# Performance work log

Measured on AMD Instinct MI355X. Metric: run time of the kernel, lower is better.

## Reference

```python
import jax, jax.numpy as jnp
import numpy as np

B, T, C = 8, 2048, 512   # batch, seq_len, channels (= output_size for residual)
H, K, D = 4, 128, 128    # heads, key_size, per-head value size
KS, DIL = 4, 4           # conv kernel size, dilation = kernal_size**block_id
BAND = 3                 # matrix_band_part num_lower = num_upper = 3
NEG = -10000000.0


def setup_inputs() -> dict:
    key = jax.random.key(0)
    ks = jax.random.split(key, 12)
    s = 0.02
    f32 = jnp.float32
    x = jax.random.normal(ks[0], (B, T, C), f32)
    # per-head q/k/v dense params (stacked over head axis)
    Wq = jax.random.normal(ks[1], (H, C, K), f32) * s
    bq = jnp.zeros((H, K), f32)
    Wk = jax.random.normal(ks[2], (H, C, K), f32) * s
    bk = jnp.zeros((H, K), f32)
    Wv = jax.random.normal(ks[3], (H, C, D), f32) * s
    bv = jnp.zeros((H, D), f32)
    # output combiner Dense(output_size)
    Wo = jax.random.normal(ks[4], (H * D, C), f32) * s
    bo = jnp.zeros((C,), f32)
    # causal dilated Conv1D: kernel layout WIO = (kernel, in, out)
    Wc = jax.random.normal(ks[5], (KS, C, C), f32) * s
    bc = jnp.zeros((C,), f32)
    return {"x": x, "Wq": Wq, "bq": bq, "Wk": Wk, "bk": bk,
            "Wv": Wv, "bv": bv, "Wo": Wo, "bo": bo, "Wc": Wc, "bc": bc}


def reference(x, Wq, bq, Wk, bk, Wv, bv, Wo, bo, Wc, bc):
    # per-head projections: [B,H,T,K/D]
    q = jnp.einsum('btc,hck->bhtk', x, Wq) + bq[None, :, None, :]
    k = jnp.einsum('btc,hck->bhtk', x, Wk) + bk[None, :, None, :]
    v = jnp.einsum('btc,hcd->bhtd', x, Wv) + bv[None, :, None, :]
    # dense scores then band mask (faithful to matrix_band_part + abs>0 mask)
    sim = jnp.einsum('bhtk,bhsk->bhts', q, k) / jnp.sqrt(jnp.float32(K))
    idx = jnp.arange(T)
    band = (jnp.abs(idx[:, None] - idx[None, :]) <= BAND).astype(sim.dtype)
    simb = sim * band
    mask = jnp.where(jnp.abs(simb) > 0.0, 0.0, 1.0).astype(sim.dtype)
    att = jax.nn.softmax(simb + NEG * mask, axis=-1)
    heads = jnp.einsum('bhts,bhsd->bhtd', att, v)          # [B,H,T,D]
    cat = heads.transpose(0, 2, 1, 3).reshape(B, T, H * D)  # concat heads
    out = cat @ Wo + bo                                     # Dense(512)
    # causal dilated conv + relu
    pad = (KS - 1) * DIL
    conv = jax.lax.conv_general_dilated(
        out, Wc, window_strides=(1,), padding=[(pad, 0)],
        rhs_dilation=(DIL,), dimension_numbers=('NWC', 'WIO', 'NWC'))
    conv = jax.nn.relu(conv + bc)
    res = conv + x
    return jnp.where(res >= 0, res, 0.2 * res)  # leaky_relu(alpha=0.2)
```

## Files before the change

### kernel.cpp

```cpp
#include <hip/hip_runtime.h>
#include <math.h>

#define Bb    8
#define Tseq  2048
#define Cch   512
#define Mrows 16384
#define Nqkv  1536

typedef __bf16 bf16x8 __attribute__((ext_vector_type(8)));
typedef __bf16 bf16x4 __attribute__((ext_vector_type(4)));
typedef float  f32x4  __attribute__((ext_vector_type(4)));

__device__ __forceinline__ void gld_lds16(const void* g, void* l) {
  __builtin_amdgcn_global_load_lds(
      (const __attribute__((address_space(1))) unsigned int*)g,
      (__attribute__((address_space(3))) unsigned int*)l, 16, 0, 0);
}

#define SWZ(r, g) (((r) << 6) + ((((g) ^ ((r) & 7))) << 3))

__device__ __forceinline__ void swizzle_mn(int* m0, int* n0) {
  const int NX = gridDim.x;
  const int total = NX * gridDim.y;
  const int lid = blockIdx.y * NX + blockIdx.x;
  const int xcd = lid & 7;
  const int chunk = lid >> 3;
  const int idx = xcd * (total >> 3) + chunk;
  const int mt = idx / NX;
  const int nt = idx - mt * NX;
  *m0 = mt * 128;
  *n0 = nt * 128;
}

__global__ __launch_bounds__(256, 2) void gemm_qkv_wp_kernel(
    const __bf16* __restrict__ xb, const __bf16* __restrict__ Wqkv_t,
    const float* __restrict__ bq, const float* __restrict__ bk,
    const float* __restrict__ bv, __bf16* __restrict__ qkv,
    const __bf16* __restrict__ Wc_t, const __bf16* __restrict__ Wob,
    __bf16* __restrict__ Wp_bt) {
  __shared__ __align__(16) __bf16 As[2][128 * 64];
  __shared__ __align__(16) __bf16 Bs[2][128 * 64];
  const int tid = threadIdx.x;
  const int w = tid >> 6, lane = tid & 63;
  const int wm = w & 1, wn = w >> 1;
  const int lm = lane & 15, quad = lane >> 4;
  const int srow = lane >> 3;
  const int scol = (((lane & 7) ^ srow) << 3);
  const int lid = blockIdx.x;

  const __bf16 *Ap, *Bp;
  __bf16* op;
  int lda, ldo, m0, n0;
  bool dobias;
  if (lid < 1536) {
    const int xcd = lid & 7, chunk = lid >> 3;
    const int idx = xcd * 192 + chunk;
    const int mt = idx / 12, nt = idx - mt * 12;
    m0 = mt * 128; n0 = nt * 128;
    Ap = xb; lda = 512; Bp = Wqkv_t;
    op = qkv; ldo = 1536; dobias = true;
  } else {
    const int l2 = lid - 1536;
    const int z = l2 >> 4;
    m0 = ((l2 >> 2) & 3) * 128; n0 = (l2 & 3) * 128;
    Ap = Wc_t + z * 512; lda = 2048; Bp = Wob;
    op = Wp_bt + z * 512; ldo = 2048; dobias = false;
  }

  auto stage = [&](int buf, int k0) {
#pragma unroll
    for (int it = 0; it < 4; ++it) {
      const int c = w * 4 + it;
      const int row = c * 8 + srow;
      gld_lds16(Ap + (size_t)(m0 + row) * lda + k0 + scol, &As[buf][c * 512]);
      gld_lds16(Bp + (size_t)(n0 + row) * 512 + k0 + scol, &Bs[buf][c * 512]);
    }
  };

  f32x4 acc[4][4] = {};
  stage(0, 0);
  int cur = 0;
  for (int k0 = 0; k0 < 512; k0 += 64) {
    if (k0 + 64 < 512) {
      stage(cur ^ 1, k0 + 64);
      asm volatile("s_waitcnt vmcnt(8)" ::: "memory");
    } else {
      asm volatile("s_waitcnt vmcnt(0)" ::: "memory");
    }
    __builtin_amdgcn_s_barrier();
    asm volatile("" ::: "memory");
    __builtin_amdgcn_s_setprio(1);
#pragma unroll
    for (int ks = 0; ks < 2; ++ks) {
      bf16x8 af[4], bfr[4];
#pragma unroll
      for (int i = 0; i < 4; ++i)
        af[i] = *(const bf16x8*)&As[cur][SWZ(wm * 64 + i * 16 + lm, ks * 4 + quad)];
#pragma unroll
      for (int j = 0; j < 4; ++j)
        bfr[j] = *(const bf16x8*)&Bs[cur][SWZ(wn * 64 + j * 16 + lm, ks * 4 + quad)];
#pragma unroll
      for (int i = 0; i < 4; ++i)
#pragma unroll
        for (int j = 0; j < 4; ++j)
          acc[i][j] = __builtin_amdgcn_mfma_f32_16x16x32_bf16(af[i], bfr[j], acc[i][j], 0, 0, 0);
    }
    __builtin_amdgcn_s_setprio(0);
    asm volatile("" ::: "memory");
    __builtin_amdgcn_s_barrier();
    asm volatile("" ::: "memory");
    cur ^= 1;
  }
#pragma unroll
  for (int j = 0; j < 4; ++j) {
    const int col = n0 + wn * 64 + j * 16 + lm;
    float bias = 0.f;
    if (dobias) {
      const int s = col >> 9;
      const float* bp = (s == 0) ? bq : (s == 1 ? bk : bv);
      bias = bp[col & 511];
    }
#pragma unroll
    for (int i = 0; i < 4; ++i) {
      const int row0 = m0 + wm * 64 + i * 16 + quad * 4;
#pragma unroll
      for (int r = 0; r < 4; ++r)
        op[(size_t)(row0 + r) * ldo + col] = (__bf16)(acc[i][j][r] + bias);
    }
  }
}

__global__ __launch_bounds__(256, 2) void conv_gemm_kernel(
    const __bf16* __restrict__ A,
    const __bf16* __restrict__ Bt,
    const float* __restrict__ bc, const float* __restrict__ bj,
    const float* __restrict__ x, float* __restrict__ out,
    const __bf16* __restrict__ zeros) {
  __shared__ __align__(16) __bf16 As[2][128 * 64];
  __shared__ __align__(16) __bf16 Bs[2][128 * 64];
  const int tid = threadIdx.x;
  const int w = tid >> 6, lane = tid & 63;
  const int wm = w & 1, wn = w >> 1;
  const int lm = lane & 15, quad = lane >> 4;
  const int srow = lane >> 3;
  const int scol = (((lane & 7) ^ srow) << 3);
  int m0, n0;
  swizzle_mn(&m0, &n0);

  auto stage = [&](int buf, int k0) {
    const int jtap = k0 >> 9;
    const int shift = 4 * jtap - 12;
    const int cin0 = k0 & 511;
#pragma unroll
    for (int it = 0; it < 4; ++it) {
      const int c = w * 4 + it;
      const int row = c * 8 + srow;
      const int m = m0 + row;
      const __bf16* src = (((m & (Tseq - 1)) + shift) >= 0)
                              ? A + (size_t)(m + shift) * Cch + cin0 + scol
                              : zeros + scol;
      gld_lds16(src, &As[buf][c * 512]);
      gld_lds16(Bt + (size_t)(n0 + row) * 2048 + k0 + scol, &Bs[buf][c * 512]);
    }
  };

  f32x4 acc[4][4] = {};
  stage(0, 0);
  int cur = 0;
  for (int k0 = 0; k0 < 4 * Cch; k0 += 64) {
    if (k0 + 64 < 4 * Cch) {
      stage(cur ^ 1, k0 + 64);
      asm volatile("s_waitcnt vmcnt(8)" ::: "memory");
    } else {
      asm volatile("s_waitcnt vmcnt(0)" ::: "memory");
    }
    __builtin_amdgcn_s_barrier();
    asm volatile("" ::: "memory");
    __builtin_amdgcn_s_setprio(1);
#pragma unroll
    for (int ks = 0; ks < 2; ++ks) {
      bf16x8 af[4], bfr[4];
#pragma unroll
      for (int i = 0; i < 4; ++i)
        af[i] = *(const bf16x8*)&As[cur][SWZ(wm * 64 + i * 16 + lm, ks * 4 + quad)];
#pragma unroll
      for (int j = 0; j < 4; ++j)
        bfr[j] = *(const bf16x8*)&Bs[cur][SWZ(wn * 64 + j * 16 + lm, ks * 4 + quad)];
#pragma unroll
      for (int i = 0; i < 4; ++i)
#pragma unroll
        for (int j = 0; j < 4; ++j)
          acc[i][j] = __builtin_amdgcn_mfma_f32_16x16x32_bf16(af[i], bfr[j], acc[i][j], 0, 0, 0);
    }
    __builtin_amdgcn_s_setprio(0);
    asm volatile("" ::: "memory");
    __builtin_amdgcn_s_barrier();
    asm volatile("" ::: "memory");
    cur ^= 1;
  }
#pragma unroll
  for (int j = 0; j < 4; ++j) {
    const int col = n0 + wn * 64 + j * 16 + lm;
    const float bcv = bc[col];
    float suf[4];
    suf[3] = bj[3 * 512 + col];
    suf[2] = suf[3] + bj[2 * 512 + col];
    suf[1] = suf[2] + bj[1 * 512 + col];
    suf[0] = suf[1] + bj[0 * 512 + col];
#pragma unroll
    for (int i = 0; i < 4; ++i) {
      const int row0 = m0 + wm * 64 + i * 16 + quad * 4;
#pragma unroll
      for (int r = 0; r < 4; ++r) {
        const int row = row0 + r;
        const int tl = row & (Tseq - 1);
        int jm = 15 - tl;
        jm = (jm < 0) ? 0 : (jm >> 2);
        float v = acc[i][j][r] + bcv + suf[jm];
        v = fmaxf(v, 0.f);
        v += x[(size_t)row * Cch + col];
        out[(size_t)row * Cch + col] = (v >= 0.f) ? v : 0.2f * v;
      }
    }
  }
}

__global__ __launch_bounds__(256) void attn_band_kernel(
    const __bf16* __restrict__ qkv, __bf16* __restrict__ cat) {
  __shared__ __align__(16) __bf16 ks[70 * 128];
  __shared__ __align__(16) __bf16 vs[70 * 128];
  const int tid = threadIdx.x;
  const int bh = blockIdx.y;
  const int b = bh >> 2, h = bh & 3;
  const int t0 = blockIdx.x * 64;
  for (int c = tid; c < 70 * 16; c += 256) {
    const int row = c >> 4, chunk = c & 15;
    int s = t0 - 3 + row;
    s = (s < 0) ? 0 : ((s > Tseq - 1) ? Tseq - 1 : s);
    const __bf16* src = qkv + ((size_t)(b * Tseq + s)) * Nqkv + 512 + h * 128 + chunk * 8;
    *(bf16x8*)&ks[row * 128 + chunk * 8] = *(const bf16x8*)src;
    *(bf16x8*)&vs[row * 128 + chunk * 8] = *(const bf16x8*)(src + 512);
  }
  __syncthreads();
  const int g = tid & 15, grp = tid >> 4;
  const int d0 = g * 8;
  const float scale = 0.08838834764831845f;
#pragma unroll
  for (int tt = 0; tt < 4; ++tt) {
    const int tl = grp * 4 + tt;
    const int t = t0 + tl;
    bf16x8 qv = *(const bf16x8*)(qkv + ((size_t)(b * Tseq + t)) * Nqkv + h * 128 + d0);
    float score[7];
#pragma unroll
    for (int i = 0; i < 7; ++i) {
      const int s = t - 3 + i;
      const bool valid = (s >= 0) && (s < Tseq);
      bf16x8 kv = *(const bf16x8*)&ks[(tl + i) * 128 + d0];
      float p = 0.f;
#pragma unroll
      for (int e = 0; e < 8; ++e) p += (float)qv[e] * (float)kv[e];
      p += __shfl_xor(p, 1);
      p += __shfl_xor(p, 2);
      p += __shfl_xor(p, 4);
      p += __shfl_xor(p, 8);
      score[i] = valid ? p * scale : -1e30f;
    }
    float mx = score[0];
#pragma unroll
    for (int i = 1; i < 7; ++i) mx = fmaxf(mx, score[i]);
    float wgt[7], denom = 0.f;
#pragma unroll
    for (int i = 0; i < 7; ++i) {
      wgt[i] = (score[i] > -1e29f) ? expf(score[i] - mx) : 0.f;
      denom += wgt[i];
    }
    const float inv = 1.f / denom;
    float o[8] = {};
#pragma unroll
    for (int i = 0; i < 7; ++i) {
      bf16x8 vv = *(const bf16x8*)&vs[(tl + i) * 128 + d0];
#pragma unroll
      for (int e = 0; e < 8; ++e) o[e] += wgt[i] * (float)vv[e];
    }
    bf16x8 ov;
#pragma unroll
    for (int e = 0; e < 8; ++e) ov[e] = (__bf16)(o[e] * inv);
    *(bf16x8*)(cat + ((size_t)(b * Tseq + t)) * Cch + h * 128 + d0) = ov;
  }
}

#define PREP_A 8192
#define PREP_B 8960
#define PREP_C 9984
#define PREP_D 10240
#define PREP_E 10241
#define PREP_N 10273

__global__ __launch_bounds__(256) void prep_kernel(
    const float* __restrict__ x, const float* __restrict__ Wq,
    const float* __restrict__ Wk, const float* __restrict__ Wv,
    const float* __restrict__ Wo, const float* __restrict__ Wc,
    const float* __restrict__ bo,
    __bf16* __restrict__ xb, __bf16* __restrict__ Wqkv_t,
    __bf16* __restrict__ Wc_t, __bf16* __restrict__ Wob,
    float* __restrict__ bj, __bf16* __restrict__ zeros) {
  __shared__ float sArr[32][33];
  __shared__ float red[256];
  const int bid = blockIdx.x;
  const int tid = threadIdx.x;
  if (bid < PREP_A) {
    const size_t i = ((size_t)bid * 256 + tid) * 4;
    float4 v = *(const float4*)(x + i);
    bf16x4 o;
    o[0] = (__bf16)v.x; o[1] = (__bf16)v.y; o[2] = (__bf16)v.z; o[3] = (__bf16)v.w;
    *(bf16x4*)(xb + i) = o;
  } else if (bid < PREP_B) {
    const int l = bid - PREP_A;
    const int bx = l & 3, by = (l >> 2) & 15, z = l >> 6;
    const int sgrp = z >> 2, h = z & 3;
    const float* src = ((sgrp == 0) ? Wq : (sgrp == 1) ? Wk : Wv) + h * (512 * 128);
    __bf16* dst = Wqkv_t + (size_t)z * 128 * 512;
    const int tx = tid & 31, ty = tid >> 5;
    const int c0 = bx * 32, r0 = by * 32;
#pragma unroll
    for (int rr = 0; rr < 4; ++rr)
      sArr[ty + rr * 8][tx] = src[(size_t)(r0 + ty + rr * 8) * 128 + c0 + tx];
    __syncthreads();
#pragma unroll
    for (int rr = 0; rr < 4; ++rr)
      dst[(size_t)(c0 + ty + rr * 8) * 512 + r0 + tx] = (__bf16)sArr[tx][ty + rr * 8];
  } else if (bid < PREP_C) {
    const int l = bid - PREP_B;
    const int bx = l & 15, by = l >> 4;
    const int tx = tid & 31, ty = tid >> 5;
    const int c0 = bx * 32, r0 = by * 32;
#pragma unroll
    for (int rr = 0; rr < 4; ++rr)
      sArr[ty + rr * 8][tx] = Wc[(size_t)(r0 + ty + rr * 8) * 512 + c0 + tx];
    __syncthreads();
#pragma unroll
    for (int rr = 0; rr < 4; ++rr)
      Wc_t[(size_t)(c0 + ty + rr * 8) * 2048 + r0 + tx] = (__bf16)sArr[tx][ty + rr * 8];
  } else if (bid < PREP_D) {
    const int l = bid - PREP_C;
    const size_t i = ((size_t)l * 256 + tid) * 4;
    float4 v = *(const float4*)(Wo + i);
    bf16x4 o;
    o[0] = (__bf16)v.x; o[1] = (__bf16)v.y; o[2] = (__bf16)v.z; o[3] = (__bf16)v.w;
    *(bf16x4*)(Wob + i) = o;
  } else if (bid < PREP_E) {
    bf16x8 zero = {};
    *(bf16x8*)(zeros + tid * 8) = zero;
  } else {
    const int l = bid - PREP_E;
    const int j = l >> 3, nb = l & 7;
    const int n = nb * 64 + (tid & 63);
    const int cig = tid >> 6;
    const float* base = Wc + ((size_t)j * 512 + cig * 128) * 512 + n;
    float acc = 0.f;
#pragma unroll 8
    for (int ci = 0; ci < 128; ++ci) acc += bo[cig * 128 + ci] * base[(size_t)ci * 512];
    red[tid] = acc;
    __syncthreads();
    if (tid < 64)
      bj[j * 512 + n] = red[tid] + red[tid + 64] + red[tid + 128] + red[tid + 192];
  }
}

extern "C" void kernel_launch(void* const* d_in, const int* in_sizes, int n_in,
                              void* d_out, int out_size, void* d_ws, size_t ws_size,
                              hipStream_t stream) {
  const float* x  = (const float*)d_in[0];
  const float* Wq = (const float*)d_in[1];
  const float* bq = (const float*)d_in[2];
  const float* Wk = (const float*)d_in[3];
  const float* bk = (const float*)d_in[4];
  const float* Wv = (const float*)d_in[5];
  const float* bv = (const float*)d_in[6];
  const float* Wo = (const float*)d_in[7];
  const float* bo = (const float*)d_in[8];
  const float* Wc = (const float*)d_in[9];
  const float* bc = (const float*)d_in[10];
  float* out = (float*)d_out;

  char* p = (char*)d_ws;
  __bf16* xb     = (__bf16*)p;  p += (size_t)Mrows * Cch * 2;
  __bf16* qkv    = (__bf16*)p;  p += (size_t)Mrows * Nqkv * 2;
  __bf16* catb   = (__bf16*)p;  p += (size_t)Mrows * Cch * 2;
  __bf16* Wqkv_t = (__bf16*)p;  p += (size_t)Nqkv * Cch * 2;
  __bf16* Wc_t   = (__bf16*)p;  p += (size_t)Cch * 2048 * 2;
  __bf16* Wob    = (__bf16*)p;  p += (size_t)Cch * Cch * 2;
  __bf16* Wp_bt  = (__bf16*)p;  p += (size_t)Cch * 2048 * 2;
  float*  bj     = (float*)p;   p += 4 * Cch * 4;
  __bf16* zeros  = (__bf16*)p;  p += 4096;

  prep_kernel<<<PREP_N, 256, 0, stream>>>(x, Wq, Wk, Wv, Wo, Wc, bo,
                                          xb, Wqkv_t, Wc_t, Wob, bj, zeros);

  gemm_qkv_wp_kernel<<<1600, 256, 0, stream>>>(xb, Wqkv_t, bq, bk, bv, qkv,
                                               Wc_t, Wob, Wp_bt);

  attn_band_kernel<<<dim3(Tseq / 64, Bb * 4), 256, 0, stream>>>(qkv, catb);

  conv_gemm_kernel<<<dim3(Cch / 128, Mrows / 128), 256, 0, stream>>>(
      catb, Wp_bt, bc, bj, x, out, zeros);
}
```

Measured before the change: 211.5 us.

## Use 256x128 tiles with 8 waves and triple-buffered LDS pipeline in GEMMs

Result: slower. 224.7 us (+6.2%).

```diff
diff --git a/kernel.cpp b/kernel.cpp
--- a/kernel.cpp
+++ b/kernel.cpp
@@ -19,30 +19,18 @@
 
 #define SWZ(r, g) (((r) << 6) + ((((g) ^ ((r) & 7))) << 3))
 
-__device__ __forceinline__ void swizzle_mn(int* m0, int* n0) {
-  const int NX = gridDim.x;
-  const int total = NX * gridDim.y;
-  const int lid = blockIdx.y * NX + blockIdx.x;
-  const int xcd = lid & 7;
-  const int chunk = lid >> 3;
-  const int idx = xcd * (total >> 3) + chunk;
-  const int mt = idx / NX;
-  const int nt = idx - mt * NX;
-  *m0 = mt * 128;
-  *n0 = nt * 128;
-}
-
-__global__ __launch_bounds__(256, 2) void gemm_qkv_wp_kernel(
+
+__global__ __launch_bounds__(512, 2) void gemm_qkv_wp_kernel(
     const __bf16* __restrict__ xb, const __bf16* __restrict__ Wqkv_t,
     const float* __restrict__ bq, const float* __restrict__ bk,
     const float* __restrict__ bv, __bf16* __restrict__ qkv,
     const __bf16* __restrict__ Wc_t, const __bf16* __restrict__ Wob,
     __bf16* __restrict__ Wp_bt) {
-  __shared__ __align__(16) __bf16 As[2][128 * 64];
-  __shared__ __align__(16) __bf16 Bs[2][128 * 64];
+  __shared__ __align__(16) __bf16 As[3][256 * 64];
+  __shared__ __align__(16) __bf16 Bs[3][128 * 64];
   const int tid = threadIdx.x;
   const int w = tid >> 6, lane = tid & 63;
-  const int wm = w & 1, wn = w >> 1;
+  const int wm = w & 3, wn = w >> 2;
   const int lm = lane & 15, quad = lane >> 4;
   const int srow = lane >> 3;
   const int scol = (((lane & 7) ^ srow) << 3);
@@ -52,41 +40,44 @@
   __bf16* op;
   int lda, ldo, m0, n0;
   bool dobias;
-  if (lid < 1536) {
+  if (lid < 768) {
     const int xcd = lid & 7, chunk = lid >> 3;
-    const int idx = xcd * 192 + chunk;
+    const int idx = xcd * 96 + chunk;
     const int mt = idx / 12, nt = idx - mt * 12;
-    m0 = mt * 128; n0 = nt * 128;
+    m0 = mt * 256; n0 = nt * 128;
     Ap = xb; lda = 512; Bp = Wqkv_t;
     op = qkv; ldo = 1536; dobias = true;
   } else {
-    const int l2 = lid - 1536;
-    const int z = l2 >> 4;
-    m0 = ((l2 >> 2) & 3) * 128; n0 = (l2 & 3) * 128;
+    const int l2 = lid - 768;
+    const int z = l2 >> 3, rest = l2 & 7;
+    m0 = (rest >> 2) * 256; n0 = (rest & 3) * 128;
     Ap = Wc_t + z * 512; lda = 2048; Bp = Wob;
     op = Wp_bt + z * 512; ldo = 2048; dobias = false;
   }
 
-  auto stage = [&](int buf, int k0) {
+  auto stage = [&](int buf, int t) {
+    const int k0 = t * 64;
 #pragma unroll
     for (int it = 0; it < 4; ++it) {
       const int c = w * 4 + it;
-      const int row = c * 8 + srow;
-      gld_lds16(Ap + (size_t)(m0 + row) * lda + k0 + scol, &As[buf][c * 512]);
-      gld_lds16(Bp + (size_t)(n0 + row) * 512 + k0 + scol, &Bs[buf][c * 512]);
+      gld_lds16(Ap + (size_t)(m0 + c * 8 + srow) * lda + k0 + scol,
+                &As[buf][c * 512]);
+    }
+#pragma unroll
+    for (int it = 0; it < 2; ++it) {
+      const int c = w * 2 + it;
+      gld_lds16(Bp + (size_t)(n0 + c * 8 + srow) * 512 + k0 + scol,
+                &Bs[buf][c * 512]);
     }
   };
 
   f32x4 acc[4][4] = {};
   stage(0, 0);
-  int cur = 0;
-  for (int k0 = 0; k0 < 512; k0 += 64) {
-    if (k0 + 64 < 512) {
-      stage(cur ^ 1, k0 + 64);
-      asm volatile("s_waitcnt vmcnt(8)" ::: "memory");
-    } else {
-      asm volatile("s_waitcnt vmcnt(0)" ::: "memory");
-    }
+  stage(1, 1);
+  int bufc = 0;
+  for (int t = 0; t < 8; ++t) {
+    if (t < 7) asm volatile("s_waitcnt vmcnt(6)" ::: "memory");
+    else       asm volatile("s_waitcnt vmcnt(0)" ::: "memory");
     __builtin_amdgcn_s_barrier();
     asm volatile("" ::: "memory");
     __builtin_amdgcn_s_setprio(1);
@@ -95,10 +86,10 @@
       bf16x8 af[4], bfr[4];
 #pragma unroll
       for (int i = 0; i < 4; ++i)
-        af[i] = *(const bf16x8*)&As[cur][SWZ(wm * 64 + i * 16 + lm, ks * 4 + quad)];
+        af[i] = *(const bf16x8*)&As[bufc][SWZ(wm * 64 + i * 16 + lm, ks * 4 + quad)];
 #pragma unroll
       for (int j = 0; j < 4; ++j)
-        bfr[j] = *(const bf16x8*)&Bs[cur][SWZ(wn * 64 + j * 16 + lm, ks * 4 + quad)];
+        bfr[j] = *(const bf16x8*)&Bs[bufc][SWZ(wn * 64 + j * 16 + lm, ks * 4 + quad)];
 #pragma unroll
       for (int i = 0; i < 4; ++i)
 #pragma unroll
@@ -109,7 +100,11 @@
     asm volatile("" ::: "memory");
     __builtin_amdgcn_s_barrier();
     asm volatile("" ::: "memory");
-    cur ^= 1;
+    if (t + 2 < 8) {
+      int bn = bufc + 2; if (bn >= 3) bn -= 3;
+      stage(bn, t + 2);
+    }
+    ++bufc; if (bufc == 3) bufc = 0;
   }
 #pragma unroll
   for (int j = 0; j < 4; ++j) {
@@ -130,50 +125,55 @@
   }
 }
 
-__global__ __launch_bounds__(256, 2) void conv_gemm_kernel(
+__global__ __launch_bounds__(512, 2) void conv_gemm_kernel(
     const __bf16* __restrict__ A,
     const __bf16* __restrict__ Bt,
     const float* __restrict__ bc, const float* __restrict__ bj,
     const float* __restrict__ x, float* __restrict__ out,
     const __bf16* __restrict__ zeros) {
-  __shared__ __align__(16) __bf16 As[2][128 * 64];
-  __shared__ __align__(16) __bf16 Bs[2][128 * 64];
+  __shared__ __align__(16) __bf16 As[3][256 * 64];
+  __shared__ __align__(16) __bf16 Bs[3][128 * 64];
   const int tid = threadIdx.x;
   const int w = tid >> 6, lane = tid & 63;
-  const int wm = w & 1, wn = w >> 1;
+  const int wm = w & 3, wn = w >> 2;
   const int lm = lane & 15, quad = lane >> 4;
   const int srow = lane >> 3;
   const int scol = (((lane & 7) ^ srow) << 3);
-  int m0, n0;
-  swizzle_mn(&m0, &n0);
-
-  auto stage = [&](int buf, int k0) {
+  const int lid = blockIdx.y * 4 + blockIdx.x;
+  const int xcd = lid & 7, chunk = lid >> 3;
+  const int idx = xcd * 32 + chunk;
+  const int mt = idx >> 2, nt = idx & 3;
+  const int m0 = mt * 256, n0 = nt * 128;
+
+  auto stage = [&](int buf, int t) {
+    const int k0 = t * 64;
     const int jtap = k0 >> 9;
     const int shift = 4 * jtap - 12;
     const int cin0 = k0 & 511;
 #pragma unroll
     for (int it = 0; it < 4; ++it) {
       const int c = w * 4 + it;
-      const int row = c * 8 + srow;
-      const int m = m0 + row;
+      const int m = m0 + c * 8 + srow;
       const __bf16* src = (((m & (Tseq - 1)) + shift) >= 0)
                               ? A + (size_t)(m + shift) * Cch + cin0 + scol
                               : zeros + scol;
       gld_lds16(src, &As[buf][c * 512]);
-      gld_lds16(Bt + (size_t)(n0 + row) * 2048 + k0 + scol, &Bs[buf][c * 512]);
+    }
+#pragma unroll
+    for (int it = 0; it < 2; ++it) {
+      const int c = w * 2 + it;
+      gld_lds16(Bt + (size_t)(n0 + c * 8 + srow) * 2048 + k0 + scol,
+                &Bs[buf][c * 512]);
     }
   };
 
   f32x4 acc[4][4] = {};
   stage(0, 0);
-  int cur = 0;
-  for (int k0 = 0; k0 < 4 * Cch; k0 += 64) {
-    if (k0 + 64 < 4 * Cch) {
-      stage(cur ^ 1, k0 + 64);
-      asm volatile("s_waitcnt vmcnt(8)" ::: "memory");
-    } else {
-      asm volatile("s_waitcnt vmcnt(0)" ::: "memory");
-    }
+  stage(1, 1);
+  int bufc = 0;
+  for (int t = 0; t < 32; ++t) {
+    if (t < 31) asm volatile("s_waitcnt vmcnt(6)" ::: "memory");
+    else        asm volatile("s_waitcnt vmcnt(0)" ::: "memory");
     __builtin_amdgcn_s_barrier();
     asm volatile("" ::: "memory");
     __builtin_amdgcn_s_setprio(1);
@@ -182,10 +182,10 @@
       bf16x8 af[4], bfr[4];
 #pragma unroll
       for (int i = 0; i < 4; ++i)
-        af[i] = *(const bf16x8*)&As[cur][SWZ(wm * 64 + i * 16 + lm, ks * 4 + quad)];
+        af[i] = *(const bf16x8*)&As[bufc][SWZ(wm * 64 + i * 16 + lm, ks * 4 + quad)];
 #pragma unroll
       for (int j = 0; j < 4; ++j)
-        bfr[j] = *(const bf16x8*)&Bs[cur][SWZ(wn * 64 + j * 16 + lm, ks * 4 + quad)];
+        bfr[j] = *(const bf16x8*)&Bs[bufc][SWZ(wn * 64 + j * 16 + lm, ks * 4 + quad)];
 #pragma unroll
       for (int i = 0; i < 4; ++i)
 #pragma unroll
@@ -196,7 +196,11 @@
     asm volatile("" ::: "memory");
     __builtin_amdgcn_s_barrier();
     asm volatile("" ::: "memory");
-    cur ^= 1;
+    if (t + 2 < 32) {
+      int bn = bufc + 2; if (bn >= 3) bn -= 3;
+      stage(bn, t + 2);
+    }
+    ++bufc; if (bufc == 3) bufc = 0;
   }
 #pragma unroll
   for (int j = 0; j < 4; ++j) {
@@ -397,11 +401,11 @@
   prep_kernel<<<PREP_N, 256, 0, stream>>>(x, Wq, Wk, Wv, Wo, Wc, bo,
                                           xb, Wqkv_t, Wc_t, Wob, bj, zeros);
 
-  gemm_qkv_wp_kernel<<<1600, 256, 0, stream>>>(xb, Wqkv_t, bq, bk, bv, qkv,
-                                               Wc_t, Wob, Wp_bt);
+  gemm_qkv_wp_kernel<<<800, 512, 0, stream>>>(xb, Wqkv_t, bq, bk, bv, qkv,
+                                              Wc_t, Wob, Wp_bt);
 
   attn_band_kernel<<<dim3(Tseq / 64, Bb * 4), 256, 0, stream>>>(qkv, catb);
 
-  conv_gemm_kernel<<<dim3(Cch / 128, Mrows / 128), 256, 0, stream>>>(
+  conv_gemm_kernel<<<dim3(Cch / 128, Mrows / 128 / 2), 512, 0, stream>>>(
       catb, Wp_bt, bc, bj, x, out, zeros);
 }
```
